# Kernel optimization log

Hardware: AMD Instinct MI355X
Metric: run time of the kernel (lower is better)

## Reference

```python
import jax, jax.numpy as jnp
import numpy as np

M, OUT, IN = 512, 8192, 8192
BLOCK_N, BLOCK_K = 128, 128  # weight_block_size (out_block, in_block)
OB, IB = OUT // BLOCK_N, IN // BLOCK_K  # 64, 64 scale blocks


def setup_inputs() -> dict:
    key = jax.random.key(0)
    k1, k2, k3 = jax.random.split(key, 3)
    x = jax.random.normal(k1, (M, IN), dtype=jnp.float32)
    # pre-quantized int8 weight stored as (out_features, in_features)
    weight_q = jax.random.randint(k2, (OUT, IN), -127, 127, dtype=jnp.int32).astype(jnp.int8)
    # per-(out_block, in_block) dequant scales
    weight_scale = jax.random.uniform(k3, (OB, IB), dtype=jnp.float32, minval=0.01, maxval=0.02)
    return {"x": x, "weight_q": weight_q, "weight_scale": weight_scale}


def _dequant(weight_q, weight_scale):
    # (OUT, IN) int8 -> blocks (OB, BLOCK_N, IB, BLOCK_K), scale broadcast per block
    w = weight_q.astype(jnp.float32).reshape(OB, BLOCK_N, IB, BLOCK_K)
    w = w * weight_scale[:, None, :, None]
    return w.reshape(OUT, IN)


def reference(x, weight_q, weight_scale):
    # Block-dequantize then matmul: out[m, o] = sum_i x[m, i] * (wq[o, i] * scale[o//bn, i//bk])
    w = _dequant(weight_q, weight_scale)          # (OUT, IN) fp32
    out = jnp.einsum("mi,oi->mo", x, w)           # (M, OUT)
    return out
```

## Files before the change

### kernel.cpp

```cpp
#include <hip/hip_runtime.h>

#define MDIM 512
#define NDIM 8192
#define KDIM 8192

typedef float v4f __attribute__((ext_vector_type(4)));
typedef int   v4i __attribute__((ext_vector_type(4)));
typedef char  c16 __attribute__((ext_vector_type(16)));

#define GLDS16(g, l)                                                    \
  __builtin_amdgcn_global_load_lds(                                     \
      (const __attribute__((address_space(1))) void*)(g),               \
      (__attribute__((address_space(3))) void*)(l), 16, 0, 0)
#define SB __builtin_amdgcn_sched_barrier(0)

__device__ __forceinline__ int swb(int row, int g) {
  return ((row >> 1) << 7) + (((((row & 1) << 2) | g) ^ ((row >> 1) & 7)) << 4);
}

__global__ __launch_bounds__(256) void produce_kernel(
    const int* __restrict__ wq, const float* __restrict__ x,
    char* __restrict__ w8, char* __restrict__ xq, float* __restrict__ ax) {
  if (blockIdx.x < 16384) {
    const int tid = blockIdx.x * 256 + threadIdx.x;
    const int R = tid >> 9;
    const int k16 = tid & 511;
    const int* src = wq + ((size_t)R << 13) + k16 * 16;
    v4i a[4];
#pragma unroll
    for (int h = 0; h < 4; ++h) a[h] = *(const v4i*)(src + h * 4);
    c16 q;
#pragma unroll
    for (int h = 0; h < 4; ++h) {
      q[h * 4 + 0] = (char)a[h][0];
      q[h * 4 + 1] = (char)a[h][1];
      q[h * 4 + 2] = (char)a[h][2];
      q[h * 4 + 3] = (char)a[h][3];
    }
    const int nt = R >> 6, r = R & 63;
    const int kt = k16 >> 2, g = k16 & 3;
    *(c16*)(w8 + ((size_t)(nt * 128 + kt) << 12) + swb(r, g)) = q;
  } else {
    const int m = blockIdx.x - 16384;
    const int t = threadIdx.x;
    const float* row = x + ((size_t)m << 13);
    v4f v[8];
    float mx = 0.f;
#pragma unroll
    for (int i = 0; i < 8; ++i) {
      v[i] = *(const v4f*)(row + t * 32 + i * 4);
#pragma unroll
      for (int r = 0; r < 4; ++r) mx = fmaxf(mx, fabsf(v[i][r]));
    }
#pragma unroll
    for (int d = 1; d < 64; d <<= 1) mx = fmaxf(mx, __shfl_xor(mx, d));
    __shared__ float smx[4];
    if ((t & 63) == 0) smx[t >> 6] = mx;
    __syncthreads();
    mx = fmaxf(fmaxf(smx[0], smx[1]), fmaxf(smx[2], smx[3]));
    const float inv = (mx > 0.f) ? 127.f / mx : 0.f;
    if (t == 0) ax[m] = mx / 127.f;
    const int mt = m >> 7, r = m & 127;
#pragma unroll
    for (int g2 = 0; g2 < 2; ++g2) {
      c16 q;
#pragma unroll
      for (int e = 0; e < 16; ++e) {
        const int idx = g2 * 4 + (e >> 2);
        float f = fminf(fmaxf(v[idx][e & 3] * inv, -127.f), 127.f);
        q[e] = (char)__float2int_rn(f);
      }
      const int k16 = t * 2 + g2;
      const int kt = k16 >> 2, g = k16 & 3;
      *(c16*)(xq + ((size_t)(mt * 128 + kt) << 13) + swb(r, g)) = q;
    }
  }
}

template <int KS>
__global__ __launch_bounds__(256) void reduce_kernel(const float* __restrict__ p,
                                                     float* __restrict__ out) {
  const size_t i = ((size_t)blockIdx.x * 256 + threadIdx.x) * 4;
  v4f a = *(const v4f*)(p + i);
#pragma unroll
  for (int s = 1; s < KS; ++s) a += *(const v4f*)(p + (size_t)s * MDIM * NDIM + i);
  *(v4f*)(out + i) = a;
}

template <int KS>
__global__ __launch_bounds__(256, 4) void gemm_i8_kernel(
    const char* __restrict__ xq, const char* __restrict__ w8,
    const float* __restrict__ wsc, const float* __restrict__ ax,
    float* __restrict__ outp) {
  constexpr int NKT = 128 / KS;
  __shared__ char lA[2][8192];
  __shared__ char lB[2][4096];

  const int b = blockIdx.x;
  const int c = b & 7;
  const int s = b >> 3;
  const int mt = s & 3;
  const int kh = (KS > 1) ? ((s >> 2) & (KS - 1)) : 0;
  const int nt = c * 16 + ((KS > 1) ? (s >> (2 + (KS == 2 ? 1 : 2))) : (s >> 2));
  const int m0 = mt * 128, n0 = nt * 64;
  const int kt0 = kh * NKT;

  const int t = threadIdx.x;
  const int w = t >> 6, l = t & 63;
  const int wm = (w >> 1) * 64, wn = (w & 1) * 32;
  const int l15 = l & 15, q = l >> 4;

  const char* asrc = xq + ((size_t)(mt * 128 + kt0) << 13);
  const char* bsrc = w8 + ((size_t)(nt * 128 + kt0) << 12);

  v4i acc[4][2] = {};
  v4f facc[4][2] = {};

  auto issue = [&](int tt) {
    const int buf = tt & 1;
#pragma unroll
    for (int it = 0; it < 2; ++it) {
      const int ub = (it * 4 + w) * 64;
      GLDS16(asrc + ((size_t)tt << 13) + (size_t)(ub + l) * 16, &lA[buf][ub * 16]);
    }
    GLDS16(bsrc + ((size_t)tt << 12) + (size_t)(w * 64 + l) * 16, &lB[buf][w * 1024]);
  };

  issue(0);
#pragma unroll 1
  for (int tt = 0; tt < NKT; ++tt) {
    const int cur = tt & 1;
    SB;
    __builtin_amdgcn_s_barrier();
    SB;
    if (tt + 1 < NKT) issue(tt + 1);
    SB;
    if (tt + 1 < NKT)
      asm volatile("s_waitcnt vmcnt(3)" ::: "memory");
    else
      asm volatile("s_waitcnt vmcnt(0)" ::: "memory");
    SB;
    __builtin_amdgcn_s_barrier();
    SB;

    v4i af[4], bq[2];
#pragma unroll
    for (int i = 0; i < 4; ++i)
      af[i] = *(const v4i*)&lA[cur][swb(wm + i * 16 + l15, q)];
#pragma unroll
    for (int j = 0; j < 2; ++j)
      bq[j] = *(const v4i*)&lB[cur][swb(wn + j * 16 + l15, q)];
#pragma unroll
    for (int i = 0; i < 4; ++i)
#pragma unroll
      for (int j = 0; j < 2; ++j)
        acc[i][j] = __builtin_amdgcn_mfma_i32_16x16x64_i8(
            af[i], bq[j], acc[i][j], 0, 0, 0);

    if (tt & 1) {
      const float sc = wsc[(nt >> 1) * 64 + ((kt0 + tt) >> 1)];
#pragma unroll
      for (int i = 0; i < 4; ++i)
#pragma unroll
        for (int j = 0; j < 2; ++j) {
#pragma unroll
          for (int r = 0; r < 4; ++r)
            facc[i][j][r] = fmaf(sc, (float)acc[i][j][r], facc[i][j][r]);
          acc[i][j] = v4i{0, 0, 0, 0};
        }
    }
  }

  float* dst = outp + ((KS > 1) ? (size_t)kh * MDIM * NDIM : 0);
#pragma unroll
  for (int i = 0; i < 4; ++i) {
    const int mrow = m0 + wm + i * 16 + (l >> 4) * 4;
#pragma unroll
    for (int j = 0; j < 2; ++j) {
      const int ocol = n0 + wn + j * 16 + l15;
#pragma unroll
      for (int r = 0; r < 4; ++r)
        dst[(size_t)(mrow + r) * NDIM + ocol] = ax[mrow + r] * facc[i][j][r];
    }
  }
}

extern "C" void kernel_launch(void* const* d_in, const int* in_sizes, int n_in,
                              void* d_out, int out_size, void* d_ws,
                              size_t ws_size, hipStream_t stream) {
  const float* x = (const float*)d_in[0];
  const int* wq = (const int*)d_in[1];
  const float* wsc = (const float*)d_in[2];
  float* out = (float*)d_out;

  const size_t W8 = (size_t)NDIM * KDIM;
  const size_t XQ = (size_t)MDIM * KDIM;
  const size_t AX = 65536;
  const size_t PS = (size_t)MDIM * NDIM * 4;

  char* w8 = (char*)d_ws;
  char* xq = (char*)d_ws + W8;
  float* ax = (float*)((char*)d_ws + W8 + XQ);
  float* part = (float*)((char*)d_ws + W8 + XQ + AX);

  produce_kernel<<<dim3(16384 + MDIM), dim3(256), 0, stream>>>(wq, x, w8, xq, ax);

  if (ws_size >= W8 + XQ + AX + 4 * PS) {
    gemm_i8_kernel<4><<<dim3(2048), dim3(256), 0, stream>>>(xq, w8, wsc, ax, part);
    reduce_kernel<4><<<dim3((MDIM * NDIM) / (256 * 4)), dim3(256), 0, stream>>>(part, out);
  } else if (ws_size >= W8 + XQ + AX + 2 * PS) {
    gemm_i8_kernel<2><<<dim3(1024), dim3(256), 0, stream>>>(xq, w8, wsc, ax, part);
    reduce_kernel<2><<<dim3((MDIM * NDIM) / (256 * 4)), dim3(256), 0, stream>>>(part, out);
  } else {
    gemm_i8_kernel<1><<<dim3(512), dim3(256), 0, stream>>>(xq, w8, wsc, ax, out);
  }
}
```

Measured before the change: 159.2 us.

## Widen GEMM tile to 128x128 with 512-thread blocks and drop split-K 4

```diff
diff --git a/kernel.cpp b/kernel.cpp
--- a/kernel.cpp
+++ b/kernel.cpp
@@ -88,42 +88,40 @@
 }
 
 template <int KS>
-__global__ __launch_bounds__(256, 4) void gemm_i8_kernel(
+__global__ __launch_bounds__(512) void gemm_i8_kernel(
     const char* __restrict__ xq, const char* __restrict__ w8,
     const float* __restrict__ wsc, const float* __restrict__ ax,
     float* __restrict__ outp) {
   constexpr int NKT = 128 / KS;
   __shared__ char lA[2][8192];
-  __shared__ char lB[2][4096];
+  __shared__ char lB[2][8192];
 
   const int b = blockIdx.x;
   const int c = b & 7;
   const int s = b >> 3;
   const int mt = s & 3;
   const int kh = (KS > 1) ? ((s >> 2) & (KS - 1)) : 0;
-  const int nt = c * 16 + ((KS > 1) ? (s >> (2 + (KS == 2 ? 1 : 2))) : (s >> 2));
-  const int m0 = mt * 128, n0 = nt * 64;
+  const int nt2 = c * 8 + ((KS > 1) ? (s >> 3) : (s >> 2));
+  const int m0 = mt * 128, n0 = nt2 * 128;
   const int kt0 = kh * NKT;
 
   const int t = threadIdx.x;
   const int w = t >> 6, l = t & 63;
-  const int wm = (w >> 1) * 64, wn = (w & 1) * 32;
+  const int wm = (w >> 2) * 64;
+  const int wn = (w & 3) * 32;
   const int l15 = l & 15, q = l >> 4;
 
-  const char* asrc = xq + ((size_t)(mt * 128 + kt0) << 13);
-  const char* bsrc = w8 + ((size_t)(nt * 128 + kt0) << 12);
+  const char* aS = xq + ((size_t)(mt * 128 + kt0) << 13) + (size_t)(w * 64 + l) * 16;
+  const char* bS = w8 + ((size_t)((nt2 * 2 + (w >> 2)) * 128 + kt0) << 12) +
+                   (size_t)((w & 3) * 64 + l) * 16;
 
   v4i acc[4][2] = {};
   v4f facc[4][2] = {};
 
   auto issue = [&](int tt) {
     const int buf = tt & 1;
-#pragma unroll
-    for (int it = 0; it < 2; ++it) {
-      const int ub = (it * 4 + w) * 64;
-      GLDS16(asrc + ((size_t)tt << 13) + (size_t)(ub + l) * 16, &lA[buf][ub * 16]);
-    }
-    GLDS16(bsrc + ((size_t)tt << 12) + (size_t)(w * 64 + l) * 16, &lB[buf][w * 1024]);
+    GLDS16(aS + ((size_t)tt << 13), &lA[buf][w * 1024]);
+    GLDS16(bS + ((size_t)tt << 12), &lB[buf][w * 1024]);
   };
 
   issue(0);
@@ -136,7 +134,7 @@
     if (tt + 1 < NKT) issue(tt + 1);
     SB;
     if (tt + 1 < NKT)
-      asm volatile("s_waitcnt vmcnt(3)" ::: "memory");
+      asm volatile("s_waitcnt vmcnt(2)" ::: "memory");
     else
       asm volatile("s_waitcnt vmcnt(0)" ::: "memory");
     SB;
@@ -148,8 +146,10 @@
     for (int i = 0; i < 4; ++i)
       af[i] = *(const v4i*)&lA[cur][swb(wm + i * 16 + l15, q)];
 #pragma unroll
-    for (int j = 0; j < 2; ++j)
-      bq[j] = *(const v4i*)&lB[cur][swb(wn + j * 16 + l15, q)];
+    for (int j = 0; j < 2; ++j) {
+      const int rl = (wn & 63) + j * 16 + l15;
+      bq[j] = *(const v4i*)&lB[cur][(wn >> 6) * 4096 + swb(rl, q)];
+    }
 #pragma unroll
     for (int i = 0; i < 4; ++i)
 #pragma unroll
@@ -158,7 +158,7 @@
             af[i], bq[j], acc[i][j], 0, 0, 0);
 
     if (tt & 1) {
-      const float sc = wsc[(nt >> 1) * 64 + ((kt0 + tt) >> 1)];
+      const float sc = wsc[nt2 * 64 + ((kt0 + tt) >> 1)];
 #pragma unroll
       for (int i = 0; i < 4; ++i)
 #pragma unroll
@@ -205,13 +205,10 @@
 
   produce_kernel<<<dim3(16384 + MDIM), dim3(256), 0, stream>>>(wq, x, w8, xq, ax);
 
-  if (ws_size >= W8 + XQ + AX + 4 * PS) {
-    gemm_i8_kernel<4><<<dim3(2048), dim3(256), 0, stream>>>(xq, w8, wsc, ax, part);
-    reduce_kernel<4><<<dim3((MDIM * NDIM) / (256 * 4)), dim3(256), 0, stream>>>(part, out);
-  } else if (ws_size >= W8 + XQ + AX + 2 * PS) {
-    gemm_i8_kernel<2><<<dim3(1024), dim3(256), 0, stream>>>(xq, w8, wsc, ax, part);
+  if (ws_size >= W8 + XQ + AX + 2 * PS) {
+    gemm_i8_kernel<2><<<dim3(512), dim3(512), 0, stream>>>(xq, w8, wsc, ax, part);
     reduce_kernel<2><<<dim3((MDIM * NDIM) / (256 * 4)), dim3(256), 0, stream>>>(part, out);
   } else {
-    gemm_i8_kernel<1><<<dim3(512), dim3(256), 0, stream>>>(xq, w8, wsc, ax, out);
-  }
-}
+    gemm_i8_kernel<1><<<dim3(256), dim3(512), 0, stream>>>(xq, w8, wsc, ax, out);
+  }
+}
```

After: 139.0 us. 1.15x faster.
